# Kernel tuning notes

Measured on AMD Instinct MI355X. Metric: run time of the kernel, lower is better.

Reference implementation:

```python
import jax, jax.numpy as jnp
import numpy as np

DIM = 768
HEADS = 8

def setup_inputs() -> dict:
    key = jax.random.key(0)
    k1, k2, k3, k4 = jax.random.split(key, 4)
    x = jax.random.normal(k1, (4, 2048, DIM), dtype=jnp.float32)
    # torch Linear(D, 3D, bias=False): weight [3D, D]; store transposed [D, 3D]
    W_qkv = jax.random.normal(k2, (DIM, 3 * DIM), dtype=jnp.float32) * (DIM ** -0.5)
    W_o = jax.random.normal(k3, (DIM, DIM), dtype=jnp.float32) * (DIM ** -0.5)
    b_o = jax.random.normal(k4, (DIM,), dtype=jnp.float32) * 0.01
    return {"x": x, "W_qkv": W_qkv, "W_o": W_o, "b_o": b_o}

def reference(x, W_qkv, W_o, b_o):
    B, N, D = x.shape
    H = HEADS
    dh = D // H
    scale = dh ** -0.5
    qkv = x @ W_qkv                                   # [B, N, 3D]
    qkv = qkv.reshape(B, N, 3, H, dh)
    qkv = jnp.transpose(qkv, (2, 0, 3, 1, 4))         # [3, B, H, N, dh]
    Q, K, V = qkv[0], qkv[1], qkv[2]
    scores = jnp.einsum('bhqd,bhkd->bhqk', Q, K) * scale  # [B, H, N, N]
    attn = jax.nn.softmax(scores, axis=-1)
    out = jnp.einsum('bhqk,bhkd->bhqd', attn, V)      # [B, H, N, dh]
    # Faithful to original: reshape [B,H,N,dh] -> [B,N,D] WITHOUT head transpose
    out = out.reshape(B, N, D)
    return out @ W_o + b_o
```

## Files before the change

### kernel.cpp

```cpp
#include <hip/hip_runtime.h>

typedef __attribute__((ext_vector_type(8))) short short8;
typedef __attribute__((ext_vector_type(4))) float f32x4;
typedef __attribute__((ext_vector_type(4))) _Float16 half4;
typedef __attribute__((ext_vector_type(8))) _Float16 half8;
typedef __attribute__((ext_vector_type(2))) __fp16 fp16x2;

#define B_SZ 4
#define NSEQ 2048
#define DIM  768
#define NH   8
#define DH   96

__device__ __forceinline__ unsigned short f2bf(float f) {
  unsigned int u = __float_as_uint(f);
  u += 0x7fffu + ((u >> 16) & 1u);
  return (unsigned short)(u >> 16);
}

__device__ __forceinline__ float fexp2(float x) {
#if __has_builtin(__builtin_amdgcn_exp2f)
  return __builtin_amdgcn_exp2f(x);
#else
  return exp2f(x);
#endif
}

__device__ __forceinline__ void glds16(const void* g, void* l) {
  __builtin_amdgcn_global_load_lds((const __attribute__((address_space(1))) void*)g,
                                   (__attribute__((address_space(3))) void*)l, 16, 0, 0);
}

__global__ __launch_bounds__(256) void prep_kernel(
    const float* __restrict__ x, unsigned short* __restrict__ xb,
    const float* __restrict__ Wqkv, unsigned short* __restrict__ wqkvT,
    const float* __restrict__ Wo, unsigned short* __restrict__ woT)
{
  int blk = blockIdx.x;
  if (blk < 6144) {
    int i = blk * 256 + threadIdx.x;
    float4 v = ((const float4*)x)[i];
    ushort4 o;
    o.x = f2bf(v.x); o.y = f2bf(v.y); o.z = f2bf(v.z); o.w = f2bf(v.w);
    ((ushort4*)xb)[i] = o;
    return;
  }
  __shared__ float tile[32][33];
  const float* W; unsigned short* WT; int ncols, bx, by;
  if (blk < 7872) { int r = blk - 6144; W = Wqkv; WT = wqkvT; ncols = 2304; bx = r % 72; by = r / 72; }
  else            { int r = blk - 7872; W = Wo;   WT = woT;   ncols = 768;  bx = r % 24; by = r / 24; }
  int tx = threadIdx.x & 31, ty = threadIdx.x >> 5;
  int c0 = bx * 32, r0 = by * 32;
#pragma unroll
  for (int i = 0; i < 4; i++)
    tile[ty + i * 8][tx] = W[(size_t)(r0 + ty + i * 8) * ncols + c0 + tx];
  __syncthreads();
#pragma unroll
  for (int i = 0; i < 4; i++)
    WT[(size_t)(c0 + ty + i * 8) * 768 + r0 + tx] = f2bf(tile[tx][ty + i * 8]);
}

template <int EPI>
__global__ __launch_bounds__(256) void gemm_bt(
    const unsigned short* __restrict__ A, const unsigned short* __restrict__ Bt,
    unsigned short* __restrict__ qo, unsigned short* __restrict__ ko,
    _Float16* __restrict__ vo, float* __restrict__ fo,
    const float* __restrict__ bias)
{
  __shared__ unsigned short As[128 * 32];
  __shared__ unsigned short Bs[128 * 32];
  const int t = threadIdx.x;
  const int w = t >> 6, lane = t & 63;
  const int l15 = lane & 15, qd = lane >> 4;
  const int asw = (l15 >> 1) & 3;
  const int m0 = blockIdx.y * 128, n0 = blockIdx.x * 128;
  const int wm = (w >> 1) * 64, wn = (w & 1) * 64;

  const int sr = lane >> 2;
  const int sc = ((lane & 3) ^ ((sr >> 1) & 3)) * 8;
  const unsigned short* ga = A  + (size_t)(m0 + w * 16 + sr) * DIM + sc;
  const unsigned short* gb = Bt + (size_t)(n0 + w * 16 + sr) * DIM + sc;

  f32x4 acc[4][4] = {};

  for (int k0 = 0; k0 < DIM; k0 += 32) {
    glds16(ga + k0,            &As[w * 512]);
    glds16(ga + 64 * DIM + k0, &As[(4 + w) * 512]);
    glds16(gb + k0,            &Bs[w * 512]);
    glds16(gb + 64 * DIM + k0, &Bs[(4 + w) * 512]);
    __syncthreads();
    short8 af[4], bfr[4];
#pragma unroll
    for (int i = 0; i < 4; i++)
      af[i]  = *(const short8*)&As[(wm + i * 16 + l15) * 32 + (qd ^ asw) * 8];
#pragma unroll
    for (int i = 0; i < 4; i++)
      bfr[i] = *(const short8*)&Bs[(wn + i * 16 + l15) * 32 + (qd ^ asw) * 8];
#pragma unroll
    for (int mi = 0; mi < 4; mi++)
#pragma unroll
      for (int ni = 0; ni < 4; ni++)
        acc[mi][ni] = __builtin_amdgcn_mfma_f32_16x16x32_bf16(af[mi], bfr[ni], acc[mi][ni], 0, 0, 0);
    __syncthreads();
  }

#pragma unroll
  for (int mi = 0; mi < 4; mi++)
#pragma unroll
    for (int ni = 0; ni < 4; ni++) {
      int rowb = m0 + wm + mi * 16 + qd * 4;
      int col  = n0 + wn + ni * 16 + l15;
      if (EPI == 0) {
        int b = rowb >> 11, n = rowb & 2047;
        int s = col / DIM;
        int rem = col - s * DIM;
        int hh = rem / DH;
        int c = rem - hh * DH;
        size_t bh = (size_t)(b * NH + hh);
        if (s == 2) {
          half4 pk;
#pragma unroll
          for (int r = 0; r < 4; r++) pk[r] = (_Float16)acc[mi][ni][r];
          *(half4*)&vo[(bh * DH + c) * NSEQ + n] = pk;
        } else if (s == 0) {
#pragma unroll
          for (int r = 0; r < 4; r++)
            qo[(bh * NSEQ + n + r) * DH + c] = f2bf(acc[mi][ni][r] * 0.1472444679f);
        } else {
#pragma unroll
          for (int r = 0; r < 4; r++)
            ko[(bh * NSEQ + n + r) * DH + c] = f2bf(acc[mi][ni][r]);
        }
      } else {
#pragma unroll
        for (int r = 0; r < 4; r++)
          fo[(size_t)(rowb + r) * DIM + col] = acc[mi][ni][r] + bias[col];
      }
    }
}

__global__ __launch_bounds__(256, 2) void flash_kernel(
    const unsigned short* __restrict__ Qb, const unsigned short* __restrict__ Kb,
    const _Float16* __restrict__ Vtb, unsigned short* __restrict__ Z)
{
  __shared__ unsigned char smem[49152];
  unsigned short* Qs  = (unsigned short*)smem;
  unsigned short* Ks0 = (unsigned short*)smem;
  _Float16*       Vs0 = (_Float16*)(smem + 12288);
  unsigned short* Ks1 = (unsigned short*)(smem + 24576);
  _Float16*       Vs1 = (_Float16*)(smem + 36864);

  const int t = threadIdx.x, w = t >> 6, lane = t & 63;
  const int l15 = lane & 15, qd = lane >> 4;
  const int swz = (l15 >> 1) & 3;
  const int vswz = l15 & 7;
  const int qt = blockIdx.x, h = blockIdx.y, b = blockIdx.z;
  const size_t bh = (size_t)(b * NH + h);
  const unsigned short* Qg = Qb + (bh * NSEQ + (size_t)qt * 128) * DH;
  const unsigned short* Kg = Kb + bh * NSEQ * DH;
  const _Float16*       Vg = Vtb + bh * (size_t)DH * NSEQ;

  int qoff[6];
#pragma unroll
  for (int i = 0; i < 6; i++) {
    int L = i * 256 + t;
    int r = L / 12, c = L - r * 12;
    qoff[i] = r * 96 + ((c ^ ((r >> 1) & 3)) * 8);
  }
  int koff[3];
#pragma unroll
  for (int i = 0; i < 3; i++) {
    int L = w * 192 + i * 64 + lane;
    int r = L / 12, c = L - r * 12;
    int fk = r >> 4, m = r & 15;
    int key = 32 * (fk & 1) + 4 * (fk >> 1) + 8 * (m >> 2) + (m & 3);
    koff[i] = key * 96 + ((c ^ ((r >> 1) & 3)) * 8);
  }
  int voff[3];
#pragma unroll
  for (int i = 0; i < 3; i++) {
    int L = i * 256 + t;
    int r = L >> 3, c = L & 7;
    voff[i] = r * NSEQ + ((c ^ (r & 7)) * 8);
  }

#pragma unroll
  for (int i = 0; i < 6; i++)
    glds16(Qg + qoff[i], &Qs[i * 2048 + w * 512]);
  __syncthreads();
  short8 qa[2][3];
#pragma unroll
  for (int fq = 0; fq < 2; fq++)
#pragma unroll
    for (int ks = 0; ks < 3; ks++)
      qa[fq][ks] = *(const short8*)&Qs[(w * 32 + fq * 16 + l15) * 96 + ((ks * 4 + qd) ^ swz) * 8];
  __syncthreads();

#pragma unroll
  for (int i = 0; i < 3; i++)
    glds16(Kg + koff[i], &Ks0[w * 1536 + i * 512]);
#pragma unroll
  for (int i = 0; i < 3; i++)
    glds16(Vg + voff[i], &Vs0[(i * 256 + w * 64) * 8]);

  f32x4 o[2][7] = {};
  float mprev[2] = {-1e30f, -1e30f};
  const half8 onef = {(_Float16)1.f, (_Float16)1.f, (_Float16)1.f, (_Float16)1.f,
                      (_Float16)1.f, (_Float16)1.f, (_Float16)1.f, (_Float16)1.f};

  for (int kt = 0; kt < 32; kt++) {
    __syncthreads();
    const unsigned short* Ks = (kt & 1) ? Ks1 : Ks0;
    const _Float16*       Vs = (kt & 1) ? Vs1 : Vs0;
    if (kt + 1 < 32) {
      unsigned short* Ksn = (kt & 1) ? Ks0 : Ks1;
      _Float16*       Vsn = (kt & 1) ? Vs0 : Vs1;
      const unsigned short* Kt = Kg + (size_t)(kt + 1) * 64 * DH;
      const _Float16*       Vt = Vg + (kt + 1) * 64;
#pragma unroll
      for (int i = 0; i < 3; i++)
        glds16(Kt + koff[i], &Ksn[w * 1536 + i * 512]);
#pragma unroll
      for (int i = 0; i < 3; i++)
        glds16(Vt + voff[i], &Vsn[(i * 256 + w * 64) * 8]);
    }

    f32x4 s[2][4] = {};
#pragma unroll
    for (int ks = 0; ks < 3; ks++)
#pragma unroll
      for (int fk = 0; fk < 4; fk++) {
        short8 kf = *(const short8*)&Ks[(fk * 16 + l15) * 96 + ((ks * 4 + qd) ^ swz) * 8];
        s[0][fk] = __builtin_amdgcn_mfma_f32_16x16x32_bf16(kf, qa[0][ks], s[0][fk], 0, 0, 0);
        s[1][fk] = __builtin_amdgcn_mfma_f32_16x16x32_bf16(kf, qa[1][ks], s[1][fk], 0, 0, 0);
      }

#pragma unroll
    for (int fq = 0; fq < 2; fq++) {
      float mx = fmaxf(fmaxf(s[fq][0][0], s[fq][0][1]), fmaxf(s[fq][0][2], s[fq][0][3]));
#pragma unroll
      for (int fk = 1; fk < 4; fk++)
        mx = fmaxf(mx, fmaxf(fmaxf(s[fq][fk][0], s[fq][fk][1]), fmaxf(s[fq][fk][2], s[fq][fk][3])));
      mx = fmaxf(mx, __shfl_xor(mx, 16, 64));
      mx = fmaxf(mx, __shfl_xor(mx, 32, 64));
      float mnew = fmaxf(mprev[fq], mx);
      float alpha = fexp2(mprev[fq] - mnew);
      mprev[fq] = mnew;

      half4 pf[4];
#pragma unroll
      for (int fk = 0; fk < 4; fk++) {
        union { fp16x2 h2[2]; half4 h4; } u;
        u.h2[0] = __builtin_amdgcn_cvt_pkrtz(fexp2(s[fq][fk][0] - mnew), fexp2(s[fq][fk][1] - mnew));
        u.h2[1] = __builtin_amdgcn_cvt_pkrtz(fexp2(s[fq][fk][2] - mnew), fexp2(s[fq][fk][3] - mnew));
        pf[fk] = u.h4;
      }
#pragma unroll
      for (int i = 0; i < 7; i++) o[fq][i] = o[fq][i] * alpha;

#pragma unroll
      for (int p = 0; p < 2; p++) {
        union { half4 h4[2]; half8 h8; } bu;
        bu.h4[0] = pf[p]; bu.h4[1] = pf[p + 2];
#pragma unroll
        for (int fc = 0; fc < 6; fc++) {
          half8 vf = *(const half8*)&Vs[(fc * 16 + l15) * 64 + ((p * 4 + qd) ^ vswz) * 8];
          o[fq][fc] = __builtin_amdgcn_mfma_f32_16x16x32_f16(vf, bu.h8, o[fq][fc], 0, 0, 0);
        }
        o[fq][6] = __builtin_amdgcn_mfma_f32_16x16x32_f16(onef, bu.h8, o[fq][6], 0, 0, 0);
      }
    }
  }

#pragma unroll
  for (int fq = 0; fq < 2; fq++) {
    float inv = 1.0f / o[fq][6][0];
    int q = qt * 128 + w * 32 + fq * 16 + l15;
    size_t zbase = ((size_t)b * NSEQ + h * 256 + (q >> 3)) * DIM + (q & 7) * DH;
#pragma unroll
    for (int fc = 0; fc < 6; fc++)
#pragma unroll
      for (int r = 0; r < 4; r += 2) {
        unsigned int pkd = (unsigned int)f2bf(o[fq][fc][r] * inv)
                         | ((unsigned int)f2bf(o[fq][fc][r + 1] * inv) << 16);
        *(unsigned int*)&Z[zbase + fc * 16 + qd * 4 + r] = pkd;
      }
  }
}

extern "C" void kernel_launch(void* const* d_in, const int* in_sizes, int n_in,
                              void* d_out, int out_size, void* d_ws, size_t ws_size,
                              hipStream_t stream)
{
  (void)in_sizes; (void)n_in; (void)out_size; (void)ws_size;
  const float* x    = (const float*)d_in[0];
  const float* Wqkv = (const float*)d_in[1];
  const float* Wo   = (const float*)d_in[2];
  const float* bo   = (const float*)d_in[3];
  float* out = (float*)d_out;

  unsigned short* ws    = (unsigned short*)d_ws;
  unsigned short* xb    = ws;
  unsigned short* wqkvT = xb    + (size_t)8192 * 768;
  unsigned short* woT   = wqkvT + (size_t)2304 * 768;
  unsigned short* Qw    = woT   + (size_t)768 * 768;
  unsigned short* Kw    = Qw    + (size_t)6291456;
  _Float16*       Vw    = (_Float16*)(Kw + (size_t)6291456);
  unsigned short* Zw    = (unsigned short*)(Vw + (size_t)6291456);

  prep_kernel<<<8448, 256, 0, stream>>>(x, xb, Wqkv, wqkvT, Wo, woT);
  gemm_bt<0><<<dim3(18, 64), 256, 0, stream>>>(xb, wqkvT, Qw, Kw, Vw, nullptr, nullptr);
  flash_kernel<<<dim3(16, 8, 4), 256, 0, stream>>>(Qw, Kw, Vw, Zw);
  gemm_bt<1><<<dim3(6, 64), 256, 0, stream>>>(Zw, woT, nullptr, nullptr, nullptr, out, bo);
}
```

Before: 223.7 us.

## Widen GEMM K-tile to 64 and drop flash K/V double buffering

The GEMM now stages 64-wide K slices per iteration with a new 8-way XOR swizzle, halving the number of barrier pairs per output tile while doubling LDS use. The flash kernel drops its K/V double buffer and loads each tile synchronously before computing on it, halving shared memory to 24 KB. The smaller footprint may allow more resident blocks, but it gives up the overlap of the next tile's global loads with the current tile's MFMA and softmax work.

```diff
diff --git a/kernel.cpp b/kernel.cpp
--- a/kernel.cpp
+++ b/kernel.cpp
@@ -67,40 +67,51 @@
     _Float16* __restrict__ vo, float* __restrict__ fo,
     const float* __restrict__ bias)
 {
-  __shared__ unsigned short As[128 * 32];
-  __shared__ unsigned short Bs[128 * 32];
+  __shared__ unsigned short As[128 * 64];
+  __shared__ unsigned short Bs[128 * 64];
   const int t = threadIdx.x;
   const int w = t >> 6, lane = t & 63;
   const int l15 = lane & 15, qd = lane >> 4;
-  const int asw = (l15 >> 1) & 3;
+  const int rsw = l15 & 7;
   const int m0 = blockIdx.y * 128, n0 = blockIdx.x * 128;
   const int wm = (w >> 1) * 64, wn = (w & 1) * 64;
 
-  const int sr = lane >> 2;
-  const int sc = ((lane & 3) ^ ((sr >> 1) & 3)) * 8;
-  const unsigned short* ga = A  + (size_t)(m0 + w * 16 + sr) * DIM + sc;
-  const unsigned short* gb = Bt + (size_t)(n0 + w * 16 + sr) * DIM + sc;
+  int off[2];
+#pragma unroll
+  for (int j = 0; j < 2; j++) {
+    int cl = j * 64 + lane;
+    int r16 = cl >> 3, c = cl & 7;
+    off[j] = r16 * DIM + ((c ^ (r16 & 7)) * 8);
+  }
+  const unsigned short* ga = A  + (size_t)(m0 + w * 16) * DIM;
+  const unsigned short* gb = Bt + (size_t)(n0 + w * 16) * DIM;
 
   f32x4 acc[4][4] = {};
 
-  for (int k0 = 0; k0 < DIM; k0 += 32) {
-    glds16(ga + k0,            &As[w * 512]);
-    glds16(ga + 64 * DIM + k0, &As[(4 + w) * 512]);
-    glds16(gb + k0,            &Bs[w * 512]);
-    glds16(gb + 64 * DIM + k0, &Bs[(4 + w) * 512]);
+  for (int k0 = 0; k0 < DIM; k0 += 64) {
+#pragma unroll
+    for (int j = 0; j < 2; j++) {
+      glds16(ga + k0 + off[j],            &As[w * 1024 + j * 512]);
+      glds16(ga + 64 * DIM + k0 + off[j], &As[4096 + w * 1024 + j * 512]);
+      glds16(gb + k0 + off[j],            &Bs[w * 1024 + j * 512]);
+      glds16(gb + 64 * DIM + k0 + off[j], &Bs[4096 + w * 1024 + j * 512]);
+    }
     __syncthreads();
-    short8 af[4], bfr[4];
-#pragma unroll
-    for (int i = 0; i < 4; i++)
-      af[i]  = *(const short8*)&As[(wm + i * 16 + l15) * 32 + (qd ^ asw) * 8];
-#pragma unroll
-    for (int i = 0; i < 4; i++)
-      bfr[i] = *(const short8*)&Bs[(wn + i * 16 + l15) * 32 + (qd ^ asw) * 8];
-#pragma unroll
-    for (int mi = 0; mi < 4; mi++)
-#pragma unroll
-      for (int ni = 0; ni < 4; ni++)
-        acc[mi][ni] = __builtin_amdgcn_mfma_f32_16x16x32_bf16(af[mi], bfr[ni], acc[mi][ni], 0, 0, 0);
+#pragma unroll
+    for (int ks = 0; ks < 2; ks++) {
+      short8 af[4], bfr[4];
+#pragma unroll
+      for (int i = 0; i < 4; i++)
+        af[i]  = *(const short8*)&As[(wm + i * 16 + l15) * 64 + (((ks * 4 + qd) ^ rsw)) * 8];
+#pragma unroll
+      for (int i = 0; i < 4; i++)
+        bfr[i] = *(const short8*)&Bs[(wn + i * 16 + l15) * 64 + (((ks * 4 + qd) ^ rsw)) * 8];
+#pragma unroll
+      for (int mi = 0; mi < 4; mi++)
+#pragma unroll
+        for (int ni = 0; ni < 4; ni++)
+          acc[mi][ni] = __builtin_amdgcn_mfma_f32_16x16x32_bf16(af[mi], bfr[ni], acc[mi][ni], 0, 0, 0);
+    }
     __syncthreads();
   }
 
@@ -143,12 +154,10 @@
     const unsigned short* __restrict__ Qb, const unsigned short* __restrict__ Kb,
     const _Float16* __restrict__ Vtb, unsigned short* __restrict__ Z)
 {
-  __shared__ unsigned char smem[49152];
-  unsigned short* Qs  = (unsigned short*)smem;
-  unsigned short* Ks0 = (unsigned short*)smem;
-  _Float16*       Vs0 = (_Float16*)(smem + 12288);
-  unsigned short* Ks1 = (unsigned short*)(smem + 24576);
-  _Float16*       Vs1 = (_Float16*)(smem + 36864);
+  __shared__ unsigned char smem[24576];
+  unsigned short* Qs = (unsigned short*)smem;
+  unsigned short* Ks = (unsigned short*)smem;
+  _Float16*       Vs = (_Float16*)(smem + 12288);
 
   const int t = threadIdx.x, w = t >> 6, lane = t & 63;
   const int l15 = lane & 15, qd = lane >> 4;
@@ -194,14 +203,6 @@
 #pragma unroll
     for (int ks = 0; ks < 3; ks++)
       qa[fq][ks] = *(const short8*)&Qs[(w * 32 + fq * 16 + l15) * 96 + ((ks * 4 + qd) ^ swz) * 8];
-  __syncthreads();
-
-#pragma unroll
-  for (int i = 0; i < 3; i++)
-    glds16(Kg + koff[i], &Ks0[w * 1536 + i * 512]);
-#pragma unroll
-  for (int i = 0; i < 3; i++)
-    glds16(Vg + voff[i], &Vs0[(i * 256 + w * 64) * 8]);
 
   f32x4 o[2][7] = {};
   float mprev[2] = {-1e30f, -1e30f};
@@ -210,20 +211,15 @@
 
   for (int kt = 0; kt < 32; kt++) {
     __syncthreads();
-    const unsigned short* Ks = (kt & 1) ? Ks1 : Ks0;
-    const _Float16*       Vs = (kt & 1) ? Vs1 : Vs0;
-    if (kt + 1 < 32) {
-      unsigned short* Ksn = (kt & 1) ? Ks0 : Ks1;
-      _Float16*       Vsn = (kt & 1) ? Vs0 : Vs1;
-      const unsigned short* Kt = Kg + (size_t)(kt + 1) * 64 * DH;
-      const _Float16*       Vt = Vg + (kt + 1) * 64;
-#pragma unroll
-      for (int i = 0; i < 3; i++)
-        glds16(Kt + koff[i], &Ksn[w * 1536 + i * 512]);
-#pragma unroll
-      for (int i = 0; i < 3; i++)
-        glds16(Vt + voff[i], &Vsn[(i * 256 + w * 64) * 8]);
-    }
+    const unsigned short* Kt = Kg + (size_t)kt * 64 * DH;
+#pragma unroll
+    for (int i = 0; i < 3; i++)
+      glds16(Kt + koff[i], &Ks[w * 1536 + i * 512]);
+    const _Float16* Vt = Vg + kt * 64;
+#pragma unroll
+    for (int i = 0; i < 3; i++)
+      glds16(Vt + voff[i], &Vs[(i * 256 + w * 64) * 8]);
+    __syncthreads();
 
     f32x4 s[2][4] = {};
 #pragma unroll
```

After: 219.8 us. About the same (-1.8%).
